# Performance work log

Measured on AMD Instinct MI355X. Metric: run time of the kernel, lower is better.

The kernel has to match this reference:

```python
import jax, jax.numpy as jnp
from jax import lax
import numpy as np

LSTM = 128      # encoder hidden per direction
H2 = 2 * LSTM   # decoder hidden / bi-encoder output dim
E = 1024        # embedding dim
V = 30611       # vocab
A = 64          # attention dim
B, S, T = 16, 400, 96
START_TOK = 101


def setup_inputs() -> dict:
    key = jax.random.key(0)
    ks = jax.random.split(key, 24)
    d = {}
    d["word_embedding"] = jax.random.normal(ks[0], (V, E), jnp.float32) * 0.05
    d["article"] = jax.random.randint(ks[1], (B, S), 0, V)
    d["article_length"] = jax.random.randint(ks[2], (B,), S // 2, S + 1)
    d["abstract"] = jax.random.randint(ks[3], (B, T), 0, V)

    def p(k, shape, scale):
        return jax.random.normal(k, shape, jnp.float32) * scale

    # encoder BiLSTM (PyTorch gate order i,f,g,o), forward and backward dirs
    d["enc_Wih_f"] = p(ks[4], (4 * LSTM, E), 0.03)
    d["enc_Whh_f"] = p(ks[5], (4 * LSTM, LSTM), 0.08)
    d["enc_b_f"] = jnp.zeros((4 * LSTM,), jnp.float32)
    d["enc_Wih_b"] = p(ks[6], (4 * LSTM, E), 0.03)
    d["enc_Whh_b"] = p(ks[7], (4 * LSTM, LSTM), 0.08)
    d["enc_b_b"] = jnp.zeros((4 * LSTM,), jnp.float32)
    # decoder LSTM: input = embed(1024) + context(256)
    d["dec_Wih"] = p(ks[8], (4 * H2, E + H2), 0.03)
    d["dec_Whh"] = p(ks[9], (4 * H2, H2), 0.06)
    d["dec_b"] = jnp.zeros((4 * H2,), jnp.float32)
    # vocab prediction
    d["pred_W"] = p(ks[10], (V, H2), 0.06)
    d["pred_b"] = jnp.zeros((V,), jnp.float32)
    # additive attention
    d["attn_s_W"] = p(ks[11], (A, H2), 0.06)
    d["attn_s_b"] = jnp.zeros((A,), jnp.float32)
    d["attn_h_W"] = p(ks[12], (A, H2), 0.06)
    d["attn_h_b"] = jnp.zeros((A,), jnp.float32)
    d["attn_f_W"] = p(ks[13], (1, A), 0.12)
    d["attn_f_b"] = jnp.zeros((1,), jnp.float32)
    return d


def _lstm_cell(x, h, c, Wih, Whh, b):
    g = x @ Wih.T + h @ Whh.T + b
    i, f, gg, o = jnp.split(g, 4, axis=-1)
    c = jax.nn.sigmoid(f) * c + jax.nn.sigmoid(i) * jnp.tanh(gg)
    h = jax.nn.sigmoid(o) * jnp.tanh(c)
    return h, c


def reference(word_embedding, article, article_length, abstract,
              enc_Wih_f, enc_Whh_f, enc_b_f, enc_Wih_b, enc_Whh_b, enc_b_b,
              dec_Wih, dec_Whh, dec_b, pred_W, pred_b,
              attn_s_W, attn_s_b, attn_h_W, attn_h_b, attn_f_W, attn_f_b):
    dt = word_embedding.dtype
    # ---- encoder ----
    xe = word_embedding[article]          # [B,S,E]
    xs = xe.transpose(1, 0, 2)            # [S,B,E]
    z = jnp.zeros((B, LSTM), dt)

    def fstep(carry, x):
        h, c = carry
        h, c = _lstm_cell(x, h, c, enc_Wih_f, enc_Whh_f, enc_b_f)
        return (h, c), h

    def bstep(carry, x):
        h, c = carry
        h, c = _lstm_cell(x, h, c, enc_Wih_b, enc_Whh_b, enc_b_b)
        return (h, c), h

    (hf, cf_f), out_f = lax.scan(fstep, (z, z), xs)
    (hb, cf_b), out_b = lax.scan(bstep, (z, z), xs, reverse=True)
    enc_out = jnp.concatenate([out_f, out_b], axis=-1).transpose(1, 0, 2)  # [B,S,2H]

    # decoder init state = concat of final fwd/bwd encoder states
    h0 = jnp.concatenate([hf, hb], axis=-1)   # [B,H2]
    c0 = jnp.concatenate([cf_f, cf_b], axis=-1)

    # attention mask: (+9999 valid, -9999 pad); min(score, mask) keeps valid scores
    length = jnp.clip(article_length, 1, S)
    pos = jnp.arange(S)
    mask = jnp.where(pos[None, :] < length[:, None], 9999.0, -9999.0).astype(dt)

    enc_ws = enc_out @ attn_s_W.T + attn_s_b  # [B,S,A], precomputed per original code

    # teacher forcing inputs: step 0 uses token 101, step t uses abstract[:, t-1]
    tokens_in = jnp.concatenate(
        [jnp.full((B, 1), START_TOK, dtype=abstract.dtype), abstract[:, :-1]], axis=1)
    emb_in = word_embedding[tokens_in].transpose(1, 0, 2)  # [T,B,E]

    def dstep(carry, emb):
        h, c, ctx = carry
        x = jnp.concatenate([emb, ctx], axis=-1)           # [B,E+H2]
        h, c = _lstm_cell(x, h, c, dec_Wih, dec_Whh, dec_b)
        logits = h @ pred_W.T + pred_b                     # [B,V]
        wh = h @ attn_h_W.T + attn_h_b                     # [B,A]
        score = jnp.tanh(enc_ws + wh[:, None, :]) @ attn_f_W[0] + attn_f_b[0]  # [B,S]
        score = jnp.minimum(score, mask)
        w = jax.nn.softmax(score, axis=-1)
        ctx = jnp.einsum('bs,bsd->bd', w, enc_out)         # [B,H2]
        return (h, c, ctx), logits

    ctx0 = jnp.zeros((B, H2), dt)
    _, logits = lax.scan(dstep, (h0, c0, ctx0), emb_in)    # [T,B,V]

    logits = logits.transpose(1, 0, 2).reshape(B * T, V)
    tgt = abstract.reshape(-1)
    logp = jax.nn.log_softmax(logits, axis=-1)
    nll = -jnp.take_along_axis(logp, tgt[:, None], axis=1)[:, 0]
    valid = (tgt != 0).astype(logits.dtype)                # ignore_index=0
    loss = jnp.sum(nll * valid) / jnp.maximum(jnp.sum(valid), 1.0)
    return loss
```

## Files before the change

### kernel.cpp

```cpp
#include <hip/hip_runtime.h>
#include <cmath>

#define NB 16
#define SS 400
#define TT 96
#define HL 128
#define HH 256
#define AA 64
#define VV 30611
#define VVP 30720
#define START_TOK 101
#define NCHUNK 120

typedef __attribute__((ext_vector_type(8))) short bf16x8;
typedef __attribute__((ext_vector_type(4))) float f32x4;

#define PIN4(v) asm volatile("" : "+v"((v).x), "+v"((v).y), "+v"((v).z), "+v"((v).w))
#define LBAR() asm volatile("s_waitcnt lgkmcnt(0)\n\ts_barrier" ::: "memory")

__device__ __forceinline__ float gload(const float* p) {
  return __hip_atomic_load(p, __ATOMIC_RELAXED, __HIP_MEMORY_SCOPE_AGENT);
}
__device__ __forceinline__ void gstore(float* p, float v) {
  __hip_atomic_store(p, v, __ATOMIC_RELAXED, __HIP_MEMORY_SCOPE_AGENT);
}
__device__ __forceinline__ float sigmf(float x) { return 1.0f / (1.0f + __expf(-x)); }
__device__ __forceinline__ float tanhf_(float x) {
  float xc = fminf(fmaxf(x, -15.0f), 15.0f);
  return 1.0f - 2.0f / (__expf(2.0f * xc) + 1.0f);
}
__device__ __forceinline__ short f2bf(float f) {
  unsigned u = __float_as_uint(f);
  unsigned r = (u + 0x7FFFu + ((u >> 16) & 1u)) >> 16;
  return (short)r;
}
__device__ __forceinline__ void flagbar(int* flags, int b, int g, int target) {
  __syncthreads();
  if (threadIdx.x == 0)
    __hip_atomic_store(&flags[b*8 + g], target, __ATOMIC_RELAXED, __HIP_MEMORY_SCOPE_AGENT);
  if (threadIdx.x < 8) {
    while (__hip_atomic_load(&flags[b*8 + threadIdx.x], __ATOMIC_RELAXED, __HIP_MEMORY_SCOPE_AGENT) < target)
      __builtin_amdgcn_s_sleep(1);
  }
  LBAR();
}

__global__ __launch_bounds__(256) void k_init(int* flags) {
  if (threadIdx.x < 128) flags[threadIdx.x] = 0;
}

__global__ __launch_bounds__(256) void k_casts(
    const float* __restrict__ predW, const float* __restrict__ wf,
    const float* __restrict__ wb, const float* __restrict__ dwih,
    short* __restrict__ predWb, short* __restrict__ wfB,
    short* __restrict__ wbB, short* __restrict__ dwB)
{
  const int stride = gridDim.x * 256;
  const int t0 = blockIdx.x * 256 + threadIdx.x;
  for (int i = t0; i < VVP*256; i += stride)
    predWb[i] = (i < VV*256) ? f2bf(predW[i]) : (short)0;
  for (int i = t0; i < 512*1024; i += stride) wfB[i] = f2bf(wf[i]);
  for (int i = t0; i < 512*1024; i += stride) wbB[i] = f2bf(wb[i]);
  for (int i = t0; i < 1024*1024; i += stride) {
    int r = i >> 10, k = i & 1023;
    dwB[i] = f2bf(dwih[r*1280 + k]);
  }
}

__global__ __launch_bounds__(256) void k_embproj_enc_mfma(
    const float* __restrict__ emb, const int* __restrict__ article,
    const short* __restrict__ wfB, const short* __restrict__ wbB,
    const float* __restrict__ bf, const float* __restrict__ bb,
    float* __restrict__ xcomb)
{
  const int m0 = blockIdx.x * 64;
  const int n0 = blockIdx.y * 256;
  const int t = threadIdx.x;
  const int w = t >> 6, l = t & 63;
  __shared__ short Abuf[64*136];
  __shared__ int tok[64];
  if (t < 64) {
    int R = m0 + t, s = R >> 4, b = R & 15;
    tok[t] = article[b*SS + s];
  }
  const short* __restrict__ Wb = (n0 < 512) ? wfB : wbB;
  const int nb0 = (n0 < 512) ? n0 : (n0 - 512);
  f32x4 acc[4][4];
  #pragma unroll
  for (int i = 0; i < 4; ++i)
    #pragma unroll
    for (int j = 0; j < 4; ++j) acc[i][j] = (f32x4){0.f,0.f,0.f,0.f};
  __syncthreads();
  const int ar = t >> 2, ak0 = (t & 3) * 32;
  for (int kc = 0; kc < 8; ++kc) {
    const float* src = emb + (size_t)tok[ar]*1024 + kc*128 + ak0;
    #pragma unroll
    for (int j = 0; j < 8; ++j) {
      float4 v = *(const float4*)(src + 4*j);
      short4 s4; s4.x = f2bf(v.x); s4.y = f2bf(v.y); s4.z = f2bf(v.z); s4.w = f2bf(v.w);
      *(short4*)(&Abuf[ar*136 + ak0 + 4*j]) = s4;
    }
    LBAR();
    #pragma unroll
    for (int ks = 0; ks < 4; ++ks) {
      bf16x8 af[4];
      #pragma unroll
      for (int mr = 0; mr < 4; ++mr)
        af[mr] = *(const bf16x8*)(&Abuf[(mr*16 + (l & 15))*136 + ks*32 + (l >> 4)*8]);
      #pragma unroll
      for (int ct = 0; ct < 4; ++ct) {
        int n = nb0 + w*64 + ct*16 + (l & 15);
        bf16x8 bfr = *(const bf16x8*)(Wb + (size_t)n*1024 + kc*128 + ks*32 + (l >> 4)*8);
        #pragma unroll
        for (int mr = 0; mr < 4; ++mr)
          acc[mr][ct] = __builtin_amdgcn_mfma_f32_16x16x32_bf16(af[mr], bfr, acc[mr][ct], 0, 0, 0);
      }
    }
    LBAR();
  }
  #pragma unroll
  for (int ct = 0; ct < 4; ++ct) {
    int n = n0 + w*64 + ct*16 + (l & 15);
    float bias = (n < 512) ? bf[n] : bb[n - 512];
    #pragma unroll
    for (int mr = 0; mr < 4; ++mr) {
      #pragma unroll
      for (int r = 0; r < 4; ++r) {
        int R = m0 + mr*16 + (l >> 4)*4 + r;
        xcomb[(size_t)R*1024 + n] = acc[mr][ct][r] + bias;
      }
    }
  }
}

__global__ __launch_bounds__(256) void k_embproj_dec_mfma(
    const float* __restrict__ emb, const int* __restrict__ abstr,
    const short* __restrict__ dwB, const float* __restrict__ db,
    float* __restrict__ decpre)
{
  const int m0 = blockIdx.x * 64;
  const int n0 = blockIdx.y * 256;
  const int t = threadIdx.x;
  const int w = t >> 6, l = t & 63;
  __shared__ short Abuf[64*136];
  __shared__ int tok[64];
  if (t < 64) {
    int R = m0 + t, tt = R >> 4, b = R & 15;
    tok[t] = (tt == 0) ? START_TOK : abstr[b*TT + tt - 1];
  }
  f32x4 acc[4][4];
  #pragma unroll
  for (int i = 0; i < 4; ++i)
    #pragma unroll
    for (int j = 0; j < 4; ++j) acc[i][j] = (f32x4){0.f,0.f,0.f,0.f};
  __syncthreads();
  const int ar = t >> 2, ak0 = (t & 3) * 32;
  for (int kc = 0; kc < 8; ++kc) {
    const float* src = emb + (size_t)tok[ar]*1024 + kc*128 + ak0;
    #pragma unroll
    for (int j = 0; j < 8; ++j) {
      float4 v = *(const float4*)(src + 4*j);
      short4 s4; s4.x = f2bf(v.x); s4.y = f2bf(v.y); s4.z = f2bf(v.z); s4.w = f2bf(v.w);
      *(short4*)(&Abuf[ar*136 + ak0 + 4*j]) = s4;
    }
    LBAR();
    #pragma unroll
    for (int ks = 0; ks < 4; ++ks) {
      bf16x8 af[4];
      #pragma unroll
      for (int mr = 0; mr < 4; ++mr)
        af[mr] = *(const bf16x8*)(&Abuf[(mr*16 + (l & 15))*136 + ks*32 + (l >> 4)*8]);
      #pragma unroll
      for (int ct = 0; ct < 4; ++ct) {
        int n = n0 + w*64 + ct*16 + (l & 15);
        bf16x8 bfr = *(const bf16x8*)(dwB + (size_t)n*1024 + kc*128 + ks*32 + (l >> 4)*8);
        #pragma unroll
        for (int mr = 0; mr < 4; ++mr)
          acc[mr][ct] = __builtin_amdgcn_mfma_f32_16x16x32_bf16(af[mr], bfr, acc[mr][ct], 0, 0, 0);
      }
    }
    LBAR();
  }
  #pragma unroll
  for (int ct = 0; ct < 4; ++ct) {
    int n = n0 + w*64 + ct*16 + (l & 15);
    float bias = db[n];
    #pragma unroll
    for (int mr = 0; mr < 4; ++mr) {
      #pragma unroll
      for (int r = 0; r < 4; ++r) {
        int R = m0 + mr*16 + (l >> 4)*4 + r;
        decpre[(size_t)R*1024 + n] = acc[mr][ct][r] + bias;
      }
    }
  }
}

__global__ __launch_bounds__(1024, 4) void k_encoder(
    const float* __restrict__ xcomb,
    const float* __restrict__ whhf, const float* __restrict__ whhb,
    float* __restrict__ encout,
    float* __restrict__ hpub,
    float* __restrict__ c0buf)
{
  const int b = blockIdx.x & 15, dir = blockIdx.x >> 4;
  const int t = threadIdx.x;
  const int row = t & 511;
  const int ks = t >> 9;
  const float* __restrict__ Whh = dir ? whhb : whhf;
  float4 wr[16];
  #pragma unroll
  for (int j = 0; j < 16; ++j) {
    wr[j] = *(const float4*)(Whh + row*128 + ks*64 + j*4);
    PIN4(wr[j]);
  }
  __shared__ float hl[128];
  __shared__ float part[2][512];
  float c_reg = 0.0f;
  if (t < 128) hl[t] = 0.0f;
  float xv0 = 0.f, xv1 = 0.f, xv2 = 0.f, xv3 = 0.f;
  if (t < 128) {
    const float* xr = xcomb + ((dir ? (SS-1) : 0)*NB + b)*1024 + dir*512 + t;
    xv0 = xr[0]; xv1 = xr[128]; xv2 = xr[256]; xv3 = xr[384];
  }
  __syncthreads();
  for (int s = 0; s < SS; ++s) {
    const int sf = dir ? (SS-1-s) : s;
    const float* hs = hl + ks*64;
    float a0 = 0.f, a1 = 0.f, a2 = 0.f, a3 = 0.f;
    #pragma unroll
    for (int j = 0; j < 16; j += 4) {
      float4 h0 = *(const float4*)(hs + j*4);
      float4 h1 = *(const float4*)(hs + j*4 + 4);
      float4 h2 = *(const float4*)(hs + j*4 + 8);
      float4 h3 = *(const float4*)(hs + j*4 + 12);
      a0 += wr[j].x*h0.x + wr[j].y*h0.y + wr[j].z*h0.z + wr[j].w*h0.w;
      a1 += wr[j+1].x*h1.x + wr[j+1].y*h1.y + wr[j+1].z*h1.z + wr[j+1].w*h1.w;
      a2 += wr[j+2].x*h2.x + wr[j+2].y*h2.y + wr[j+2].z*h2.z + wr[j+2].w*h2.w;
      a3 += wr[j+3].x*h3.x + wr[j+3].y*h3.y + wr[j+3].z*h3.z + wr[j+3].w*h3.w;
    }
    part[ks][row] = (a0 + a1) + (a2 + a3);
    float nx0 = 0.f, nx1 = 0.f, nx2 = 0.f, nx3 = 0.f;
    if (t < 128 && s + 1 < SS) {
      const int sfn = dir ? (SS-2-s) : (s+1);
      const float* xr = xcomb + (sfn*NB + b)*1024 + dir*512 + t;
      nx0 = xr[0]; nx1 = xr[128]; nx2 = xr[256]; nx3 = xr[384];
    }
    LBAR();
    if (t < 128) {
      float gi = part[0][t]       + part[1][t]       + xv0;
      float gf = part[0][128 + t] + part[1][128 + t] + xv1;
      float gg = part[0][256 + t] + part[1][256 + t] + xv2;
      float go = part[0][384 + t] + part[1][384 + t] + xv3;
      float iv = sigmf(gi), fv = sigmf(gf), gv = tanhf_(gg), ov = sigmf(go);
      c_reg = fv*c_reg + iv*gv;
      float hv = ov*tanhf_(c_reg);
      hl[t] = hv;
      encout[(b*SS + sf)*HH + dir*HL + t] = hv;
    }
    LBAR();
    xv0 = nx0; xv1 = nx1; xv2 = nx2; xv3 = nx3;
  }
  if (t < 128) {
    hpub[b*HH + dir*HL + t] = hl[t];
    c0buf[b*HH + dir*HL + t] = c_reg;
  }
}

__global__ __launch_bounds__(256) void k_encws(
    const float* __restrict__ encout,
    const float* __restrict__ asW, const float* __restrict__ asb,
    float* __restrict__ encwsR)
{
  const int rt = blockIdx.x;
  const int tid = threadIdx.x;
  __shared__ float Al[32*260];
  #pragma unroll
  for (int i = 0; i < 32; ++i) {
    int l = tid + i*256;
    int r = l >> 8, k = l & 255;
    Al[r*260 + k] = encout[(rt*32 + r)*256 + k];
  }
  __syncthreads();
  const int a = tid & 63, rg = tid >> 6;
  float acc[8];
  #pragma unroll
  for (int q = 0; q < 8; ++q) acc[q] = 0.0f;
  const float4* w4 = (const float4*)(asW + a*256);
  for (int k4 = 0; k4 < 64; ++k4) {
    float4 w = w4[k4];
    #pragma unroll
    for (int q = 0; q < 8; ++q) {
      const float4* a4 = (const float4*)(Al + (rg*8 + q)*260);
      float4 av = a4[k4];
      acc[q] += av.x*w.x + av.y*w.y + av.z*w.z + av.w*w.w;
    }
  }
  float bias = asb[a];
  #pragma unroll
  for (int q = 0; q < 8; ++q) {
    int row = rt*32 + rg*8 + q;
    encwsR[row*64 + a] = acc[q] + bias;
  }
}

__global__ __launch_bounds__(1024, 4) void k_decoder(
    const float* __restrict__ decpre,
    const float* __restrict__ dwhh,
    const float* __restrict__ dwih,
    const float* __restrict__ ahW, const float* __restrict__ ahb,
    const float* __restrict__ afW, const float* __restrict__ afb,
    const float* __restrict__ encwsR,
    const float* __restrict__ encout,
    const int* __restrict__ alen,
    const float* __restrict__ c0buf,
    float* hpub,
    float* cpub,
    float* wpub,
    float* __restrict__ dhall,
    int* flags)
{
  const int wg = blockIdx.x;
  const int g = wg >> 4, b = wg & 15;
  const int t = threadIdx.x;
  const int r = t & 127, ks = t >> 7;
  const int lane = t & 63;
  const int u = t & 31;
  const int s0 = g*50;

  const int grow = (r >> 5)*256 + g*32 + (r & 31);
  float4 wr[16];
  #pragma unroll
  for (int j = 0; j < 16; ++j) {
    int k = ks*64 + j*4;
    wr[j] = (k < 256) ? *(const float4*)(dwhh + grow*256 + k)
                      : *(const float4*)(dwih + grow*1280 + 1024 + (k - 256));
    PIN4(wr[j]);
  }

  __shared__ float encl[50*256];
  __shared__ float wsl[50*68];
  __shared__ float ahWt[256*68];
  __shared__ float hc[512];
  __shared__ float part[8][132];
  __shared__ float wh[64];
  __shared__ float fwl[64];
  __shared__ float scl[64];
  __shared__ float sh_m, sh_s;

  for (int i = t; i < 50*256; i += 1024) {
    int si = i >> 8, d = i & 255;
    encl[i] = encout[(b*SS + s0 + si)*HH + d];
  }
  for (int i = t; i < 50*64; i += 1024) {
    int si = i >> 6, a = i & 63;
    wsl[si*68 + a] = encwsR[(b*SS + s0 + si)*64 + a];
  }
  for (int i = t; i < 64*256; i += 1024) {
    int a = i >> 8, k = i & 255;
    ahWt[k*68 + a] = ahW[i];
  }
  if (t < 64) fwl[t] = afW[t];
  const float fb0 = afb[0];
  int len = alen[b]; len = min(max(len, 1), SS);
  float c_reg = 0.f;
  float pre0 = 0.f, pre1 = 0.f, pre2 = 0.f, pre3 = 0.f;
  if (t < 256) {
    c_reg = c0buf[b*HH + g*32 + u];
    hc[t] = gload(hpub + b*HH + t);
    hc[256 + t] = 0.0f;
    const float* pr = decpre + (size_t)(0*NB + b)*1024 + g*32 + u;
    pre0 = pr[0]; pre1 = pr[256]; pre2 = pr[512]; pre3 = pr[768];
  }
  __syncthreads();

  for (int tt = 0; tt < TT; ++tt) {
    {
      const float* hs = hc + ks*64;
      float a0 = 0.f, a1 = 0.f, a2 = 0.f, a3 = 0.f;
      #pragma unroll
      for (int j = 0; j < 16; j += 4) {
        float4 h0 = *(const float4*)(hs + j*4);
        float4 h1 = *(const float4*)(hs + j*4 + 4);
        float4 h2 = *(const float4*)(hs + j*4 + 8);
        float4 h3 = *(const float4*)(hs + j*4 + 12);
        a0 += wr[j].x*h0.x + wr[j].y*h0.y + wr[j].z*h0.z + wr[j].w*h0.w;
        a1 += wr[j+1].x*h1.x + wr[j+1].y*h1.y + wr[j+1].z*h1.z + wr[j+1].w*h1.w;
        a2 += wr[j+2].x*h2.x + wr[j+2].y*h2.y + wr[j+2].z*h2.z + wr[j+2].w*h2.w;
        a3 += wr[j+3].x*h3.x + wr[j+3].y*h3.y + wr[j+3].z*h3.z + wr[j+3].w*h3.w;
      }
      part[ks][r] = (a0 + a1) + (a2 + a3);
    }
    LBAR();
    if (t < 256) {
      float g0 = pre0, g1 = pre1, g2 = pre2, g3 = pre3;
      #pragma unroll
      for (int j = 0; j < 8; ++j) {
        g0 += part[j][u];
        g1 += part[j][32 + u];
        g2 += part[j][64 + u];
        g3 += part[j][96 + u];
      }
      float iv = sigmf(g0), fv = sigmf(g1), gv = tanhf_(g2), ov = sigmf(g3);
      c_reg = fv*c_reg + iv*gv;
      float hv = ov*tanhf_(c_reg);
      if (t < 32) {
        gstore(hpub + b*HH + g*32 + t, hv);
        dhall[(tt*NB + b)*HH + g*32 + t] = hv;
      }
      int wv = t >> 6;
      int a = wv*16 + (lane >> 2);
      int j4 = lane & 3;
      float wacc = 0.f;
      #pragma unroll
      for (int i = 0; i < 8; ++i) {
        int u2 = j4*8 + i;
        float hx = __shfl(hv, u2, 64);
        wacc += ahWt[(g*32 + u2)*68 + a] * hx;
      }
      wacc += __shfl_xor(wacc, 1);
      wacc += __shfl_xor(wacc, 2);
      if (j4 == 0) gstore(wpub + (b*8 + g)*72 + a, wacc);
    }
    flagbar(flags, b, g, 2*tt + 1);
    if (t < 256) {
      hc[t] = gload(hpub + b*HH + t);
      if (tt + 1 < TT) {
        const float* pr = decpre + (size_t)((tt+1)*NB + b)*1024 + g*32 + u;
        pre0 = pr[0]; pre1 = pr[256]; pre2 = pr[512]; pre3 = pr[768];
      }
    } else if (t < 320) {
      int a = t - 256;
      float s = ahb[a];
      #pragma unroll
      for (int j = 0; j < 8; ++j) s += gload(wpub + (b*8 + j)*72 + a);
      wh[a] = s;
    }
    LBAR();
    if (t < 800) {
      int s = t >> 4, j = t & 15;
      const float* wrow = wsl + s*68 + j*4;
      float p = fwl[j*4]   * tanhf_(wrow[0] + wh[j*4])
              + fwl[j*4+1] * tanhf_(wrow[1] + wh[j*4+1])
              + fwl[j*4+2] * tanhf_(wrow[2] + wh[j*4+2])
              + fwl[j*4+3] * tanhf_(wrow[3] + wh[j*4+3]);
      p += __shfl_xor(p, 1);
      p += __shfl_xor(p, 2);
      p += __shfl_xor(p, 4);
      p += __shfl_xor(p, 8);
      if (j == 0) scl[s] = p;
    }
    LBAR();
    if (t < 64) {
      float sc = -1e30f;
      if (t < 50) {
        sc = fb0 + scl[t];
        sc = fminf(sc, (s0 + t < len) ? 9999.0f : -9999.0f);
      }
      float m = sc;
      #pragma unroll
      for (int o = 32; o; o >>= 1) m = fmaxf(m, __shfl_xor(m, o));
      float p = (t < 50) ? __expf(sc - m) : 0.0f;
      scl[t] = p;
      float ssum = p;
      #pragma unroll
      for (int o = 32; o; o >>= 1) ssum += __shfl_xor(ssum, o);
      if (t == 0) { sh_m = m; sh_s = ssum; }
    }
    LBAR();
    if (t < 256) {
      float acc = 0.0f;
      const float* eb = encl + t;
      #pragma unroll 10
      for (int i = 0; i < 50; ++i) acc += scl[i] * eb[i*256];
      gstore(cpub + (b*8 + g)*272 + t, acc);
      if (t == 0) gstore(cpub + (b*8 + g)*272 + 256, sh_m);
      if (t == 1) gstore(cpub + (b*8 + g)*272 + 257, sh_s);
    }
    flagbar(flags, b, g, 2*tt + 2);
    if (t < 256) {
      float mj[8], sj[8];
      #pragma unroll
      for (int j = 0; j < 8; ++j) {
        mj[j] = gload(cpub + (b*8 + j)*272 + 256);
        sj[j] = gload(cpub + (b*8 + j)*272 + 257);
      }
      float M = mj[0];
      #pragma unroll
      for (int j = 1; j < 8; ++j) M = fmaxf(M, mj[j]);
      float denom = 0.f, ctx = 0.f;
      #pragma unroll
      for (int j = 0; j < 8; ++j) {
        float e = __expf(mj[j] - M);
        denom += sj[j] * e;
        ctx += gload(cpub + (b*8 + j)*272 + t) * e;
      }
      hc[256 + t] = ctx / denom;
    }
    LBAR();
  }
}

__global__ __launch_bounds__(256) void k_pred_mfma(
    const float* __restrict__ dhall,
    const short* __restrict__ predWb,
    const float* __restrict__ predb,
    float* __restrict__ pm, float* __restrict__ ps)
{
  const int m0 = blockIdx.x * 64;
  const int ch = blockIdx.y;
  const int c0 = ch * 256;
  const int t = threadIdx.x;
  const int w = t >> 6, l = t & 63;
  __shared__ __align__(16) char smem[64*264*4];
  short* Abuf = (short*)smem;
  float* L    = (float*)smem;
  __shared__ float red[256];
  __shared__ float rowmax[64];

  {
    const int ar = t >> 2, ak0 = (t & 3) * 64;
    const float* src = dhall + (size_t)(m0 + ar)*256 + ak0;
    #pragma unroll
    for (int j = 0; j < 16; ++j) {
      float4 v = *(const float4*)(src + 4*j);
      short4 s4; s4.x = f2bf(v.x); s4.y = f2bf(v.y); s4.z = f2bf(v.z); s4.w = f2bf(v.w);
      *(short4*)(&Abuf[ar*264 + ak0 + 4*j]) = s4;
    }
  }
  LBAR();
  f32x4 acc[4][4];
  #pragma unroll
  for (int i = 0; i < 4; ++i)
    #pragma unroll
    for (int j = 0; j < 4; ++j) acc[i][j] = (f32x4){0.f,0.f,0.f,0.f};
  #pragma unroll
  for (int kst = 0; kst < 8; ++kst) {
    bf16x8 af[4];
    #pragma unroll
    for (int mr = 0; mr < 4; ++mr)
      af[mr] = *(const bf16x8*)(&Abuf[(mr*16 + (l & 15))*264 + kst*32 + (l >> 4)*8]);
    #pragma unroll
    for (int ct = 0; ct < 4; ++ct) {
      int col = c0 + w*64 + ct*16 + (l & 15);
      bf16x8 bfr = *(const bf16x8*)(predWb + (size_t)col*256 + kst*32 + (l >> 4)*8);
      #pragma unroll
      for (int mr = 0; mr < 4; ++mr)
        acc[mr][ct] = __builtin_amdgcn_mfma_f32_16x16x32_bf16(af[mr], bfr, acc[mr][ct], 0, 0, 0);
    }
  }
  LBAR();
  #pragma unroll
  for (int ct = 0; ct < 4; ++ct) {
    int col = c0 + w*64 + ct*16 + (l & 15);
    float bias = (col < VV) ? predb[col] : 0.0f;
    bool valid = (col < VV);
    #pragma unroll
    for (int mr = 0; mr < 4; ++mr) {
      #pragma unroll
      for (int r = 0; r < 4; ++r) {
        int rl = mr*16 + (l >> 4)*4 + r;
        L[rl*264 + w*64 + ct*16 + (l & 15)] = valid ? (acc[mr][ct][r] + bias) : -1e30f;
      }
    }
  }
  LBAR();
  {
    const int row = t & 63, qd = t >> 6;
    float m = -1e30f;
    const float* Lr = L + row*264 + qd*64;
    for (int i = 0; i < 64; ++i) m = fmaxf(m, Lr[i]);
    red[qd*64 + row] = m;
  }
  LBAR();
  if (t < 64) {
    float m = fmaxf(fmaxf(red[t], red[64+t]), fmaxf(red[128+t], red[192+t]));
    rowmax[t] = m;
  }
  LBAR();
  {
    const int row = t & 63, qd = t >> 6;
    float m = rowmax[row];
    float ssum = 0.f;
    const float* Lr = L + row*264 + qd*64;
    for (int i = 0; i < 64; ++i) ssum += __expf(Lr[i] - m);
    red[qd*64 + row] = ssum;
  }
  LBAR();
  if (t < 64) {
    float ssum = red[t] + red[64+t] + red[128+t] + red[192+t];
    pm[(m0 + t)*NCHUNK + ch] = rowmax[t];
    ps[(m0 + t)*NCHUNK + ch] = ssum;
  }
}

__global__ __launch_bounds__(256) void k_loss_part(
    const float* __restrict__ pm, const float* __restrict__ ps,
    const float* __restrict__ dhall,
    const float* __restrict__ predW, const float* __restrict__ predb,
    const int* __restrict__ abstr, float* __restrict__ lpart)
{
  const int tid = threadIdx.x;
  const int row = blockIdx.x*256 + tid;
  __shared__ float rs[256], rc[256];
  float lsum = 0.0f, lcnt = 0.0f;
  {
    int t = row >> 4, b = row & 15;
    int tok = abstr[b*TT + t];
    float m = -1e30f;
    for (int c = 0; c < NCHUNK; ++c) m = fmaxf(m, pm[row*NCHUNK + c]);
    float ss = 0.0f;
    for (int c = 0; c < NCHUNK; ++c) ss += ps[row*NCHUNK + c] * __expf(pm[row*NCHUNK + c] - m);
    float lse = m + __logf(ss);
    float tl = predb[tok];
    const float* hrow = dhall + row*256;
    const float* wrow = predW + tok*256;
    #pragma unroll 4
    for (int k = 0; k < 256; ++k) tl += hrow[k] * wrow[k];
    if (tok != 0) { lsum = lse - tl; lcnt = 1.0f; }
  }
  rs[tid] = lsum; rc[tid] = lcnt;
  __syncthreads();
  for (int st = 128; st; st >>= 1) {
    if (tid < st) { rs[tid] += rs[tid + st]; rc[tid] += rc[tid + st]; }
    __syncthreads();
  }
  if (tid == 0) { lpart[blockIdx.x*2] = rs[0]; lpart[blockIdx.x*2 + 1] = rc[0]; }
}

__global__ void k_loss_final(const float* __restrict__ lpart, float* __restrict__ out) {
  if (threadIdx.x == 0) {
    float s = 0.f, c = 0.f;
    for (int i = 0; i < 6; ++i) { s += lpart[i*2]; c += lpart[i*2 + 1]; }
    out[0] = s / fmaxf(c, 1.0f);
  }
}

extern "C" void kernel_launch(void* const* d_in, const int* in_sizes, int n_in,
                              void* d_out, int out_size, void* d_ws, size_t ws_size,
                              hipStream_t stream) {
  const float* emb   = (const float*)d_in[0];
  const int* article = (const int*)d_in[1];
  const int* alen    = (const int*)d_in[2];
  const int* abstr   = (const int*)d_in[3];
  const float* eWihF = (const float*)d_in[4];
  const float* eWhhF = (const float*)d_in[5];
  const float* ebF   = (const float*)d_in[6];
  const float* eWihB = (const float*)d_in[7];
  const float* eWhhB = (const float*)d_in[8];
  const float* ebB   = (const float*)d_in[9];
  const float* dWih  = (const float*)d_in[10];
  const float* dWhh  = (const float*)d_in[11];
  const float* db    = (const float*)d_in[12];
  const float* pW    = (const float*)d_in[13];
  const float* pb    = (const float*)d_in[14];
  const float* asW   = (const float*)d_in[15];
  const float* asb   = (const float*)d_in[16];
  const float* ahW   = (const float*)d_in[17];
  const float* ahb   = (const float*)d_in[18];
  const float* afW   = (const float*)d_in[19];
  const float* afb   = (const float*)d_in[20];
  float* out = (float*)d_out;

  float* w = (float*)d_ws;
  size_t o = 0;
  float* xcomb  = w + o; o += (size_t)SS*NB*1024;
  float* encout = w + o; o += (size_t)NB*SS*HH;
  float* encwsR = w + o; o += (size_t)NB*SS*AA;
  float* decpre = w + o; o += (size_t)TT*NB*1024;
  float* dhall  = w + o; o += (size_t)TT*NB*HH;
  float* hpub   = w + o; o += NB*HH;
  float* cpub   = w + o; o += NB*8*272;
  float* wpub   = w + o; o += NB*8*72;
  float* c0buf  = w + o; o += NB*HH;
  float* pm     = w + o; o += (size_t)TT*NB*NCHUNK;
  float* ps     = w + o; o += (size_t)TT*NB*NCHUNK;
  float* lpart  = w + o; o += 16;
  int* flags = (int*)(w + o); o += 128;
  short* predWb = (short*)(w + o); o += (size_t)VVP*256/2;
  short* wfB    = (short*)(w + o); o += 512*1024/2;
  short* wbB    = (short*)(w + o); o += 512*1024/2;
  short* dwB    = (short*)(w + o); o += 1024*1024/2;

  k_init<<<1, 256, 0, stream>>>(flags);
  k_casts<<<2048, 256, 0, stream>>>(pW, eWihF, eWihB, dWih, predWb, wfB, wbB, dwB);
  k_embproj_enc_mfma<<<dim3(100, 4), 256, 0, stream>>>(emb, article, wfB, wbB, ebF, ebB, xcomb);
  k_embproj_dec_mfma<<<dim3(24, 4), 256, 0, stream>>>(emb, abstr, dwB, db, decpre);
  k_encoder<<<32, 1024, 0, stream>>>(xcomb, eWhhF, eWhhB, encout, hpub, c0buf);
  k_encws<<<200, 256, 0, stream>>>(encout, asW, asb, encwsR);
  k_decoder<<<128, 1024, 0, stream>>>(decpre, dWhh, dWih, ahW, ahb, afW, afb,
                                      encwsR, encout, alen, c0buf, hpub, cpub, wpub, dhall, flags);
  k_pred_mfma<<<dim3(24, 120), 256, 0, stream>>>(dhall, predWb, pb, pm, ps);
  k_loss_part<<<6, 256, 0, stream>>>(pm, ps, dhall, pW, pb, abstr, lpart);
  k_loss_final<<<1, 64, 0, stream>>>(lpart, out);
}
```

Baseline: 1.715 ms.

## Run encoder recurrence as batched bf16 MFMA in one block per direction

Replaces the per-(batch,direction) fp32 scalar LSTM encoder (32 blocks) with a kernel that uses one block per direction. Each step computes the 16x512 recurrent gate matmul for all batch rows at once with bf16 MFMA, with the recurrent weights held in registers and cast to bf16 by the cast kernel. The hidden state goes through shared memory as bf16, and each thread handles two hidden units per batch row. This cuts per-step scalar FMA work and reduction traffic, but uses only 2 CUs and brings bf16 rounding into the recurrent path over 400 steps.

After: 2.001 ms. 16.6% more time.

```diff
diff --git a/kernel.cpp b/kernel.cpp
--- a/kernel.cpp
+++ b/kernel.cpp
@@ -16,6 +16,7 @@
 typedef __attribute__((ext_vector_type(4))) float f32x4;
 
 #define PIN4(v) asm volatile("" : "+v"((v).x), "+v"((v).y), "+v"((v).z), "+v"((v).w))
+#define PINV(v) asm volatile("" : "+v"(v))
 #define LBAR() asm volatile("s_waitcnt lgkmcnt(0)\n\ts_barrier" ::: "memory")
 
 __device__ __forceinline__ float gload(const float* p) {
@@ -52,8 +53,10 @@
 __global__ __launch_bounds__(256) void k_casts(
     const float* __restrict__ predW, const float* __restrict__ wf,
     const float* __restrict__ wb, const float* __restrict__ dwih,
+    const float* __restrict__ whhf, const float* __restrict__ whhb,
     short* __restrict__ predWb, short* __restrict__ wfB,
-    short* __restrict__ wbB, short* __restrict__ dwB)
+    short* __restrict__ wbB, short* __restrict__ dwB,
+    short* __restrict__ whhfB, short* __restrict__ whhbB)
 {
   const int stride = gridDim.x * 256;
   const int t0 = blockIdx.x * 256 + threadIdx.x;
@@ -65,6 +68,8 @@
     int r = i >> 10, k = i & 1023;
     dwB[i] = f2bf(dwih[r*1280 + k]);
   }
+  for (int i = t0; i < 512*128; i += stride) whhfB[i] = f2bf(whhf[i]);
+  for (int i = t0; i < 512*128; i += stride) whhbB[i] = f2bf(whhb[i]);
 }
 
 __global__ __launch_bounds__(256) void k_embproj_enc_mfma(
@@ -196,75 +201,96 @@
   }
 }
 
-__global__ __launch_bounds__(1024, 4) void k_encoder(
+__global__ __launch_bounds__(1024, 4) void k_encoder_mfma(
     const float* __restrict__ xcomb,
-    const float* __restrict__ whhf, const float* __restrict__ whhb,
+    const short* __restrict__ whhfB, const short* __restrict__ whhbB,
     float* __restrict__ encout,
     float* __restrict__ hpub,
     float* __restrict__ c0buf)
 {
-  const int b = blockIdx.x & 15, dir = blockIdx.x >> 4;
+  const int dir = blockIdx.x;
   const int t = threadIdx.x;
-  const int row = t & 511;
-  const int ks = t >> 9;
-  const float* __restrict__ Whh = dir ? whhb : whhf;
-  float4 wr[16];
-  #pragma unroll
-  for (int j = 0; j < 16; ++j) {
-    wr[j] = *(const float4*)(Whh + row*128 + ks*64 + j*4);
-    PIN4(wr[j]);
-  }
-  __shared__ float hl[128];
-  __shared__ float part[2][512];
-  float c_reg = 0.0f;
-  if (t < 128) hl[t] = 0.0f;
-  float xv0 = 0.f, xv1 = 0.f, xv2 = 0.f, xv3 = 0.f;
-  if (t < 128) {
-    const float* xr = xcomb + ((dir ? (SS-1) : 0)*NB + b)*1024 + dir*512 + t;
-    xv0 = xr[0]; xv1 = xr[128]; xv2 = xr[256]; xv3 = xr[384];
+  const int w = t >> 6, l = t & 63;
+  const short* __restrict__ WhhB = dir ? whhbB : whhfB;
+  bf16x8 bw[2][4];
+  #pragma unroll
+  for (int nt = 0; nt < 2; ++nt)
+    #pragma unroll
+    for (int kst = 0; kst < 4; ++kst) {
+      int row = w*32 + nt*16 + (l & 15);
+      bw[nt][kst] = *(const bf16x8*)(WhhB + (size_t)row*128 + kst*32 + (l >> 4)*8);
+      PINV(bw[nt][kst]);
+    }
+  __shared__ short hbf[16*136];
+  __shared__ float gts[16*521];
+  for (int i = t; i < 16*136; i += 1024) hbf[i] = 0;
+  const int b2 = t >> 6, u = t & 63;
+  float c0r = 0.f, c1r = 0.f, h0last = 0.f, h1last = 0.f;
+  float xv[8];
+  {
+    const int sf0 = dir ? (SS-1) : 0;
+    const float* xr = xcomb + (size_t)(sf0*NB + b2)*1024 + dir*512;
+    #pragma unroll
+    for (int j = 0; j < 4; ++j) { xv[j] = xr[j*128 + u]; xv[4+j] = xr[j*128 + u + 64]; }
   }
   __syncthreads();
   for (int s = 0; s < SS; ++s) {
     const int sf = dir ? (SS-1-s) : s;
-    const float* hs = hl + ks*64;
-    float a0 = 0.f, a1 = 0.f, a2 = 0.f, a3 = 0.f;
-    #pragma unroll
-    for (int j = 0; j < 16; j += 4) {
-      float4 h0 = *(const float4*)(hs + j*4);
-      float4 h1 = *(const float4*)(hs + j*4 + 4);
-      float4 h2 = *(const float4*)(hs + j*4 + 8);
-      float4 h3 = *(const float4*)(hs + j*4 + 12);
-      a0 += wr[j].x*h0.x + wr[j].y*h0.y + wr[j].z*h0.z + wr[j].w*h0.w;
-      a1 += wr[j+1].x*h1.x + wr[j+1].y*h1.y + wr[j+1].z*h1.z + wr[j+1].w*h1.w;
-      a2 += wr[j+2].x*h2.x + wr[j+2].y*h2.y + wr[j+2].z*h2.z + wr[j+2].w*h2.w;
-      a3 += wr[j+3].x*h3.x + wr[j+3].y*h3.y + wr[j+3].z*h3.z + wr[j+3].w*h3.w;
-    }
-    part[ks][row] = (a0 + a1) + (a2 + a3);
-    float nx0 = 0.f, nx1 = 0.f, nx2 = 0.f, nx3 = 0.f;
-    if (t < 128 && s + 1 < SS) {
+    bf16x8 af[4];
+    #pragma unroll
+    for (int kst = 0; kst < 4; ++kst)
+      af[kst] = *(const bf16x8*)(&hbf[(l & 15)*136 + kst*32 + (l >> 4)*8]);
+    float nxv[8];
+    if (s + 1 < SS) {
       const int sfn = dir ? (SS-2-s) : (s+1);
-      const float* xr = xcomb + (sfn*NB + b)*1024 + dir*512 + t;
-      nx0 = xr[0]; nx1 = xr[128]; nx2 = xr[256]; nx3 = xr[384];
-    }
-    LBAR();
-    if (t < 128) {
-      float gi = part[0][t]       + part[1][t]       + xv0;
-      float gf = part[0][128 + t] + part[1][128 + t] + xv1;
-      float gg = part[0][256 + t] + part[1][256 + t] + xv2;
-      float go = part[0][384 + t] + part[1][384 + t] + xv3;
+      const float* xr = xcomb + (size_t)(sfn*NB + b2)*1024 + dir*512;
+      #pragma unroll
+      for (int j = 0; j < 4; ++j) { nxv[j] = xr[j*128 + u]; nxv[4+j] = xr[j*128 + u + 64]; }
+    }
+    f32x4 a0 = (f32x4){0.f,0.f,0.f,0.f}, a1 = (f32x4){0.f,0.f,0.f,0.f};
+    #pragma unroll
+    for (int kst = 0; kst < 4; ++kst) {
+      a0 = __builtin_amdgcn_mfma_f32_16x16x32_bf16(af[kst], bw[0][kst], a0, 0, 0, 0);
+      a1 = __builtin_amdgcn_mfma_f32_16x16x32_bf16(af[kst], bw[1][kst], a1, 0, 0, 0);
+    }
+    #pragma unroll
+    for (int r = 0; r < 4; ++r) {
+      int m = (l >> 4)*4 + r;
+      gts[m*521 + w*32 + (l & 15)] = a0[r];
+      gts[m*521 + w*32 + 16 + (l & 15)] = a1[r];
+    }
+    LBAR();
+    {
+      const float* gb = gts + b2*521;
+      float gi = gb[u]       + xv[0];
+      float gf = gb[128 + u] + xv[1];
+      float gg = gb[256 + u] + xv[2];
+      float go = gb[384 + u] + xv[3];
       float iv = sigmf(gi), fv = sigmf(gf), gv = tanhf_(gg), ov = sigmf(go);
-      c_reg = fv*c_reg + iv*gv;
-      float hv = ov*tanhf_(c_reg);
-      hl[t] = hv;
-      encout[(b*SS + sf)*HH + dir*HL + t] = hv;
-    }
-    LBAR();
-    xv0 = nx0; xv1 = nx1; xv2 = nx2; xv3 = nx3;
-  }
-  if (t < 128) {
-    hpub[b*HH + dir*HL + t] = hl[t];
-    c0buf[b*HH + dir*HL + t] = c_reg;
-  }
+      c0r = fv*c0r + iv*gv;
+      float hv0 = ov*tanhf_(c0r);
+      hbf[b2*136 + u] = f2bf(hv0);
+      encout[(size_t)(b2*SS + sf)*HH + dir*HL + u] = hv0;
+      h0last = hv0;
+      float gi2 = gb[u + 64]       + xv[4];
+      float gf2 = gb[192 + u]      + xv[5];
+      float gg2 = gb[320 + u]      + xv[6];
+      float go2 = gb[448 + u]      + xv[7];
+      float iv2 = sigmf(gi2), fv2 = sigmf(gf2), gv2 = tanhf_(gg2), ov2 = sigmf(go2);
+      c1r = fv2*c1r + iv2*gv2;
+      float hv1 = ov2*tanhf_(c1r);
+      hbf[b2*136 + u + 64] = f2bf(hv1);
+      encout[(size_t)(b2*SS + sf)*HH + dir*HL + u + 64] = hv1;
+      h1last = hv1;
+    }
+    LBAR();
+    #pragma unroll
+    for (int j = 0; j < 8; ++j) xv[j] = nxv[j];
+  }
+  hpub[b2*HH + dir*HL + u] = h0last;
+  hpub[b2*HH + dir*HL + u + 64] = h1last;
+  c0buf[b2*HH + dir*HL + u] = c0r;
+  c0buf[b2*HH + dir*HL + u + 64] = c1r;
 }
 
 __global__ __launch_bounds__(256) void k_encws(
@@ -314,9 +340,7 @@
     const float* __restrict__ encout,
     const int* __restrict__ alen,
     const float* __restrict__ c0buf,
-    float* hpub,
-    float* cpub,
-    float* wpub,
+    float* hpub, float* cpub, float* wpub,
     float* __restrict__ dhall,
     int* flags)
 {
@@ -681,12 +705,15 @@
   short* wfB    = (short*)(w + o); o += 512*1024/2;
   short* wbB    = (short*)(w + o); o += 512*1024/2;
   short* dwB    = (short*)(w + o); o += 1024*1024/2;
+  short* whhfB  = (short*)(w + o); o += 512*128/2;
+  short* whhbB  = (short*)(w + o); o += 512*128/2;
 
   k_init<<<1, 256, 0, stream>>>(flags);
-  k_casts<<<2048, 256, 0, stream>>>(pW, eWihF, eWihB, dWih, predWb, wfB, wbB, dwB);
+  k_casts<<<2048, 256, 0, stream>>>(pW, eWihF, eWihB, dWih, eWhhF, eWhhB,
+                                    predWb, wfB, wbB, dwB, whhfB, whhbB);
   k_embproj_enc_mfma<<<dim3(100, 4), 256, 0, stream>>>(emb, article, wfB, wbB, ebF, ebB, xcomb);
   k_embproj_dec_mfma<<<dim3(24, 4), 256, 0, stream>>>(emb, abstr, dwB, db, decpre);
-  k_encoder<<<32, 1024, 0, stream>>>(xcomb, eWhhF, eWhhB, encout, hpub, c0buf);
+  k_encoder_mfma<<<2, 1024, 0, stream>>>(xcomb, whhfB, whhbB, encout, hpub, c0buf);
   k_encws<<<200, 256, 0, stream>>>(encout, asW, asb, encwsR);
   k_decoder<<<128, 1024, 0, stream>>>(decpre, dWhh, dWih, ahW, ahb, afW, afb,
                                       encwsR, encout, alen, c0buf, hpub, cpub, wpub, dhall, flags);
```

## Overlap pred_W bf16 cast with encoder recurrence; shrink decoder attention weight LDS

Applied to the files above, without the earlier changes.

The conversion of the large vocab projection weight to bf16 moves out of the casts kernel and into 224 extra blocks of the encoder launch. These blocks run on otherwise idle CUs while the 32 latency-bound recurrence blocks execute. The decoder now stages only its own 32-column slice of attn_h_W in shared memory instead of the full transposed matrix, which cuts LDS use and load work per block. The risk is that the extra cast blocks compete for bandwidth with, or delay, the recurrence blocks.

Result: faster. 1.624 ms (-5.3%).

```diff
diff --git a/kernel.cpp b/kernel.cpp
--- a/kernel.cpp
+++ b/kernel.cpp
@@ -50,15 +50,12 @@
 }
 
 __global__ __launch_bounds__(256) void k_casts(
-    const float* __restrict__ predW, const float* __restrict__ wf,
-    const float* __restrict__ wb, const float* __restrict__ dwih,
-    short* __restrict__ predWb, short* __restrict__ wfB,
-    short* __restrict__ wbB, short* __restrict__ dwB)
+    const float* __restrict__ wf, const float* __restrict__ wb,
+    const float* __restrict__ dwih,
+    short* __restrict__ wfB, short* __restrict__ wbB, short* __restrict__ dwB)
 {
   const int stride = gridDim.x * 256;
   const int t0 = blockIdx.x * 256 + threadIdx.x;
-  for (int i = t0; i < VVP*256; i += stride)
-    predWb[i] = (i < VV*256) ? f2bf(predW[i]) : (short)0;
   for (int i = t0; i < 512*1024; i += stride) wfB[i] = f2bf(wf[i]);
   for (int i = t0; i < 512*1024; i += stride) wbB[i] = f2bf(wb[i]);
   for (int i = t0; i < 1024*1024; i += stride) {
@@ -201,10 +198,18 @@
     const float* __restrict__ whhf, const float* __restrict__ whhb,
     float* __restrict__ encout,
     float* __restrict__ hpub,
-    float* __restrict__ c0buf)
-{
+    float* __restrict__ c0buf,
+    const float* __restrict__ predW, short* __restrict__ predWb)
+{
+  const int t = threadIdx.x;
+  if (blockIdx.x >= 32) {
+    const size_t idx0 = (size_t)(blockIdx.x - 32) * 1024 + t;
+    const size_t stride = (size_t)224 * 1024;
+    for (size_t i = idx0; i < (size_t)VVP*256; i += stride)
+      predWb[i] = (i < (size_t)VV*256) ? f2bf(predW[i]) : (short)0;
+    return;
+  }
   const int b = blockIdx.x & 15, dir = blockIdx.x >> 4;
-  const int t = threadIdx.x;
   const int row = t & 511;
   const int ks = t >> 9;
   const float* __restrict__ Whh = dir ? whhb : whhf;
@@ -314,9 +319,7 @@
     const float* __restrict__ encout,
     const int* __restrict__ alen,
     const float* __restrict__ c0buf,
-    float* hpub,
-    float* cpub,
-    float* wpub,
+    float* hpub, float* cpub, float* wpub,
     float* __restrict__ dhall,
     int* flags)
 {
@@ -340,7 +343,7 @@
 
   __shared__ float encl[50*256];
   __shared__ float wsl[50*68];
-  __shared__ float ahWt[256*68];
+  __shared__ float ahWt[32*68];
   __shared__ float hc[512];
   __shared__ float part[8][132];
   __shared__ float wh[64];
@@ -356,9 +359,9 @@
     int si = i >> 6, a = i & 63;
     wsl[si*68 + a] = encwsR[(b*SS + s0 + si)*64 + a];
   }
-  for (int i = t; i < 64*256; i += 1024) {
-    int a = i >> 8, k = i & 255;
-    ahWt[k*68 + a] = ahW[i];
+  for (int i = t; i < 32*64; i += 1024) {
+    int u2 = i >> 6, a = i & 63;
+    ahWt[u2*68 + a] = ahW[a*HH + g*32 + u2];
   }
   if (t < 64) fwl[t] = afW[t];
   const float fb0 = afb[0];
@@ -416,7 +419,7 @@
       for (int i = 0; i < 8; ++i) {
         int u2 = j4*8 + i;
         float hx = __shfl(hv, u2, 64);
-        wacc += ahWt[(g*32 + u2)*68 + a] * hx;
+        wacc += ahWt[u2*68 + a] * hx;
       }
       wacc += __shfl_xor(wacc, 1);
       wacc += __shfl_xor(wacc, 2);
@@ -683,10 +686,10 @@
   short* dwB    = (short*)(w + o); o += 1024*1024/2;
 
   k_init<<<1, 256, 0, stream>>>(flags);
-  k_casts<<<2048, 256, 0, stream>>>(pW, eWihF, eWihB, dWih, predWb, wfB, wbB, dwB);
+  k_casts<<<512, 256, 0, stream>>>(eWihF, eWihB, dWih, wfB, wbB, dwB);
   k_embproj_enc_mfma<<<dim3(100, 4), 256, 0, stream>>>(emb, article, wfB, wbB, ebF, ebB, xcomb);
   k_embproj_dec_mfma<<<dim3(24, 4), 256, 0, stream>>>(emb, abstr, dwB, db, decpre);
-  k_encoder<<<32, 1024, 0, stream>>>(xcomb, eWhhF, eWhhB, encout, hpub, c0buf);
+  k_encoder<<<256, 1024, 0, stream>>>(xcomb, eWhhF, eWhhB, encout, hpub, c0buf, pW, predWb);
   k_encws<<<200, 256, 0, stream>>>(encout, asW, asb, encwsR);
   k_decoder<<<128, 1024, 0, stream>>>(decpre, dWhh, dWih, ahW, ahb, afW, afb,
                                       encwsR, encout, alen, c0buf, hpub, cpub, wpub, dhall, flags);
```
